# Kernel tuning notes

Measured on AMD Instinct MI355X. Metric: run time of the kernel, lower is better.

Reference implementation:

```python
import jax, jax.numpy as jnp
import numpy as np

N = 50000          # num nodes
E = 600000         # num edges
F_IN = 128         # num_features
H = 128            # graph_hidden_dim
R = 2              # num_relations
L = 3              # n_layers_conv
BN_EPS = 1e-5
BN_BETA = 1e-4     # BatchNorm bias init per module code


def setup_inputs() -> dict:
    key = jax.random.key(0)
    ks = jax.random.split(key, 9)
    s_in = 1.0 / np.sqrt(F_IN)
    s_h = 1.0 / np.sqrt(H)
    return {
        "x": jax.random.normal(ks[0], (N, F_IN), jnp.float32),
        "edge_index": jax.random.randint(ks[1], (2, E), 0, N, jnp.int32),
        "edge_type": jax.random.randint(ks[2], (E,), 0, R, jnp.int32),
        "W0_rel": jax.random.normal(ks[3], (R, F_IN, H), jnp.float32) * s_in,
        "W0_root": jax.random.normal(ks[4], (F_IN, H), jnp.float32) * s_in,
        "b0": jnp.zeros((H,), jnp.float32),
        "Ws_rel": jax.random.normal(ks[5], (L, R, H, H), jnp.float32) * s_h,
        "Ws_root": jax.random.normal(ks[6], (L, H, H), jnp.float32) * s_h,
        "bs": jnp.zeros((L, H), jnp.float32),
    }


def batchnorm(x):
    # training-mode BatchNorm1d over nodes; weight=1, bias=1e-4 (per init)
    mu = jnp.mean(x, axis=0)
    var = jnp.mean((x - mu) ** 2, axis=0)  # biased var, as torch uses for norm
    return (x - mu) * jax.lax.rsqrt(var + BN_EPS) + BN_BETA


def rgcn_conv(x, src, dst, edge_type, W_rel, W_root, b):
    # PyG RGCNConv, aggr='mean': per-relation mean of x[src] at dst,
    # then per-relation linear, plus root transform and bias.
    seg = dst * R + edge_type  # combined (node, relation) segment id
    msgs = x[src]                                   # [E, d] gather
    sums = jax.ops.segment_sum(msgs, seg, num_segments=N * R)
    cnts = jax.ops.segment_sum(jnp.ones((src.shape[0],), x.dtype), seg,
                               num_segments=N * R)
    mean = sums.reshape(N, R, -1) / jnp.maximum(cnts, 1.0).reshape(N, R, 1)
    out = jnp.einsum('nrd,rdh->nh', mean, W_rel) + x @ W_root + b
    return out


def reference(x, edge_index, edge_type, W0_rel, W0_root, b0, Ws_rel, Ws_root, bs):
    src, dst = edge_index[0], edge_index[1]
    h = batchnorm(x)
    h = jax.nn.relu(rgcn_conv(h, src, dst, edge_type, W0_rel, W0_root, b0))
    for i in range(L):
        h_ = batchnorm(h)
        h_ = jax.nn.relu(rgcn_conv(h_, src, dst, edge_type,
                                   Ws_rel[i], Ws_root[i], bs[i]))
        h = h + h_  # conv_residual=True
    return h  # gconv_dropout == 0
```

## Files before the change

kernel.cpp:

```cpp
#include <hip/hip_runtime.h>
#include <hip/hip_bf16.h>

#define N_NODES 50000
#define N_EDGES 600000
#define F 128
#define R 2
#define NLAYER 4
#define NSEG (N_NODES * R)
#define SEGP (NSEG / 8)
#define NSCB 98
#define NB 384
#define BN_EPS 1e-5f
#define BETA 1e-4f

typedef __hip_bfloat16 bf16;
typedef __attribute__((ext_vector_type(8))) short short8;
typedef __attribute__((ext_vector_type(4))) short short4x;
typedef __attribute__((ext_vector_type(4))) float floatx4;

__device__ __forceinline__ float b2f(short s) {
    union { unsigned u; float f; } c;
    c.u = ((unsigned)(unsigned short)s) << 16;
    return c.f;
}

__global__ void k_wt(const float* __restrict__ W0_rel, const float* __restrict__ W0_root,
                     const float* __restrict__ Ws_rel, const float* __restrict__ Ws_root,
                     bf16* __restrict__ Bt) {
    int idx = blockIdx.x * 256 + threadIdx.x;
    if (idx >= NLAYER * NB * F) return;
    int l = idx / (NB * F);
    int rem = idx % (NB * F);
    int j = rem / F, d = rem % F;
    float v;
    if (j < 256) {
        int r = j >> 7, c = j & 127;
        v = (l == 0) ? W0_rel[(r * F + d) * F + c]
                     : Ws_rel[((size_t)((l - 1) * R + r) * F + d) * F + c];
    } else {
        int c = j - 256;
        v = (l == 0) ? W0_root[d * F + c]
                     : Ws_root[((size_t)(l - 1) * F + d) * F + c];
    }
    Bt[idx] = __float2bfloat16(v);
}

__global__ void k_seg(const int* __restrict__ dst, const int* __restrict__ et,
                      int* __restrict__ seg) {
    int e = blockIdx.x * 256 + threadIdx.x;
    if (e < N_EDGES) seg[e] = dst[e] * R + et[e];
}

__global__ void k_count(const int* __restrict__ seg, int* __restrict__ cnt) {
    int g = blockIdx.x & 7;
    int lo = g * SEGP, hi = lo + SEGP;
    for (int e = (blockIdx.x >> 3) * 256 + threadIdx.x; e < N_EDGES; e += 65536) {
        int s = seg[e];
        if (s >= lo && s < hi) atomicAdd(&cnt[s], 1);
    }
}

__global__ void k_scan1(const int* __restrict__ cnt, int* __restrict__ off,
                        int* __restrict__ bsum) {
    int t = threadIdx.x;
    int g = blockIdx.x * 1024 + t;
    int v = (g < NSEG) ? cnt[g] : 0;
    int lane = t & 63;
    int wv = t >> 6;
    int x = v;
    for (int d = 1; d < 64; d <<= 1) {
        int y = __shfl_up(x, d, 64);
        if (lane >= d) x += y;
    }
    __shared__ int wtot[16];
    if (lane == 63) wtot[wv] = x;
    __syncthreads();
    if (t < 16) {
        int s = wtot[t];
        for (int d = 1; d < 16; d <<= 1) {
            int y = __shfl_up(s, d, 64);
            if (t >= d) s += y;
        }
        wtot[t] = s;
    }
    __syncthreads();
    int wpre = (wv == 0) ? 0 : wtot[wv - 1];
    int incl = x + wpre;
    if (g < NSEG) off[g] = incl - v;
    if (t == 1023) bsum[blockIdx.x] = incl;
}

__global__ void k_scan2(int* __restrict__ bsum) {
    __shared__ int s[128];
    int t = threadIdx.x;
    int v = (t < NSCB) ? bsum[t] : 0;
    s[t] = v;
    __syncthreads();
    for (int d = 1; d < 128; d <<= 1) {
        int y = (t >= d) ? s[t - d] : 0;
        __syncthreads();
        s[t] += y;
        __syncthreads();
    }
    if (t < NSCB) bsum[t] = s[t] - v;
}

__global__ void k_scan3(int* __restrict__ off, const int* __restrict__ bsum) {
    int g = blockIdx.x * 1024 + threadIdx.x;
    if (g < NSEG) off[g] += bsum[blockIdx.x];
}

__global__ void k_fill(const int* __restrict__ src, const int* __restrict__ seg,
                       const int* __restrict__ off,
                       int* __restrict__ fill, int* __restrict__ esrc) {
    int g = blockIdx.x & 7;
    int lo = g * SEGP, hi = lo + SEGP;
    for (int e = (blockIdx.x >> 3) * 256 + threadIdx.x; e < N_EDGES; e += 65536) {
        int s = seg[e];
        if (s >= lo && s < hi) {
            int idx = off[s] + atomicAdd(&fill[s], 1);
            esrc[idx] = src[e];
        }
    }
}

__global__ void k_bnstats(const float* __restrict__ h, float* __restrict__ gs) {
    int c = threadIdx.x & 127;
    int rl = threadIdx.x >> 7;
    float s = 0.f, q = 0.f;
    for (int r = blockIdx.x * 2 + rl; r < N_NODES; r += gridDim.x * 2) {
        float v = h[(size_t)r * F + c];
        s += v; q += v * v;
    }
    __shared__ float ls[256], lq[256];
    ls[threadIdx.x] = s; lq[threadIdx.x] = q;
    __syncthreads();
    if (rl == 0) {
        atomicAdd(&gs[c], ls[c] + ls[c + 128]);
        atomicAdd(&gs[128 + c], lq[c] + lq[c + 128]);
    }
}

__launch_bounds__(512)
__global__ void k_gemm(const float* __restrict__ h, const float* __restrict__ gs,
                       const bf16* __restrict__ Bt, const float* __restrict__ bias,
                       bf16* __restrict__ y, bf16* __restrict__ z) {
    __shared__ bf16 As[64 * 136];
    __shared__ bf16 Bs[128 * 136];
    int t = threadIdx.x;
    int m0 = blockIdx.x * 64;
    int c4 = (t & 31) * 4;
    float mu[4], rs[4];
    for (int c = 0; c < 4; c++) {
        float mm = gs[c4 + c] * (1.0f / N_NODES);
        float qq = gs[128 + c4 + c] * (1.0f / N_NODES);
        mu[c] = mm;
        rs[c] = rsqrtf(qq - mm * mm + BN_EPS);
    }
    int r0 = t >> 5;
    for (int it = 0; it < 4; it++) {
        int row = r0 + it * 16;
        int m = m0 + row;
        float4 v = {0.f, 0.f, 0.f, 0.f};
        if (m < N_NODES) v = *(const float4*)(h + (size_t)m * F + c4);
        bf16 o[4];
        o[0] = __float2bfloat16((v.x - mu[0]) * rs[0] + BETA);
        o[1] = __float2bfloat16((v.y - mu[1]) * rs[1] + BETA);
        o[2] = __float2bfloat16((v.z - mu[2]) * rs[2] + BETA);
        o[3] = __float2bfloat16((v.w - mu[3]) * rs[3] + BETA);
        *(double*)(As + row * 136 + c4) = *(const double*)o;
    }
    __syncthreads();
    int w = t >> 6;
    int lane = t & 63;
    int msub = w & 3;
    int nh = w >> 2;
    int lm = lane & 15;
    int lq = lane >> 4;
    short8 a[4];
    for (int ki = 0; ki < 4; ki++)
        a[ki] = *(const short8*)(As + (msub * 16 + lm) * 136 + ki * 32 + lq * 8);
    int m = m0 + msub * 16 + lm;
    for (int ci = 0; ci < 3; ci++) {
        __syncthreads();
        {
            const bf16* bsrc = Bt + (size_t)ci * 128 * F;
            for (int rr = 0; rr < 4; rr++) {
                int idx = rr * 512 + t;
                int row = idx >> 4;
                int kc = idx & 15;
                short8 v = *(const short8*)(bsrc + row * F + kc * 8);
                *(short8*)(Bs + row * 136 + kc * 8) = v;
            }
        }
        __syncthreads();
        for (int tt = 0; tt < 4; tt++) {
            int nt = nh * 4 + tt;
            short8 b[4];
            for (int ki = 0; ki < 4; ki++)
                b[ki] = *(const short8*)(Bs + (nt * 16 + lm) * 136 + ki * 32 + lq * 8);
            floatx4 acc = {0.f, 0.f, 0.f, 0.f};
            for (int ki = 0; ki < 4; ki++)
                acc = __builtin_amdgcn_mfma_f32_16x16x32_bf16(b[ki], a[ki], acc, 0, 0, 0);
            int n0 = ci * 128 + nt * 16 + lq * 4;
            if (m < N_NODES) {
                if (ci < 2) {
                    union { bf16 o[4]; double d; } u;
                    u.o[0] = __float2bfloat16(acc[0]);
                    u.o[1] = __float2bfloat16(acc[1]);
                    u.o[2] = __float2bfloat16(acc[2]);
                    u.o[3] = __float2bfloat16(acc[3]);
                    *(double*)(y + (size_t)m * 256 + n0) = u.d;
                } else {
                    float4 bv = *(const float4*)(bias + (n0 - 256));
                    union { bf16 o[4]; double d; } u;
                    u.o[0] = __float2bfloat16(acc[0] + bv.x);
                    u.o[1] = __float2bfloat16(acc[1] + bv.y);
                    u.o[2] = __float2bfloat16(acc[2] + bv.z);
                    u.o[3] = __float2bfloat16(acc[3] + bv.w);
                    *(double*)(z + (size_t)m * F + (n0 - 256)) = u.d;
                }
            }
        }
    }
}

__global__ void k_aggregate(const bf16* __restrict__ y, const bf16* __restrict__ z,
                            const int* __restrict__ cnt, const int* __restrict__ off,
                            const int* __restrict__ esrc,
                            const float* __restrict__ hres, float* __restrict__ hout,
                            int layer) {
    int wid = (blockIdx.x * 256 + threadIdx.x) >> 6;
    int lane = threadIdx.x & 63;
    if (wid >= N_NODES) return;
    int n = wid;
    int half = lane >> 5;
    int hl = lane & 31;
    int c4 = hl * 4;
    int2 cc = *(const int2*)(cnt + n * R);
    int o0 = off[n * R];
    int myc = half ? cc.y : cc.x;
    int myo = half ? (o0 + cc.x) : o0;
    float myinv = (myc > 0) ? 1.0f / (float)myc : 0.f;
    const bf16* yb = y + half * 128 + c4;
    float s0 = 0.f, s1 = 0.f, s2 = 0.f, s3 = 0.f;
    for (int i = 0; i < myc; i += 8) {
        int sn[8];
        #pragma unroll
        for (int k = 0; k < 8; k++) {
            int valid = (i + k < myc);
            sn[k] = esrc[valid ? (myo + i + k) : myo];
        }
        short4x p[8];
        #pragma unroll
        for (int k = 0; k < 8; k++)
            p[k] = *(const short4x*)(yb + (size_t)sn[k] * 256);
        #pragma unroll
        for (int k = 0; k < 8; k++) {
            float wk = (i + k < myc) ? myinv : 0.f;
            s0 = fmaf(b2f(p[k].x), wk, s0);
            s1 = fmaf(b2f(p[k].y), wk, s1);
            s2 = fmaf(b2f(p[k].z), wk, s2);
            s3 = fmaf(b2f(p[k].w), wk, s3);
        }
    }
    float t0 = __shfl_xor(s0, 32, 64);
    float t1 = __shfl_xor(s1, 32, 64);
    float t2 = __shfl_xor(s2, 32, 64);
    float t3 = __shfl_xor(s3, 32, 64);
    if (half == 0) {
        short4x zb = *(const short4x*)(z + (size_t)n * F + c4);
        float4 hp = {0.f, 0.f, 0.f, 0.f};
        if (layer > 0) hp = *(const float4*)(hres + (size_t)n * F + c4);
        float4 o4;
        o4.x = fmaxf(b2f(zb.x) + s0 + t0, 0.f) + hp.x;
        o4.y = fmaxf(b2f(zb.y) + s1 + t1, 0.f) + hp.y;
        o4.z = fmaxf(b2f(zb.z) + s2 + t2, 0.f) + hp.z;
        o4.w = fmaxf(b2f(zb.w) + s3 + t3, 0.f) + hp.w;
        *(float4*)(hout + (size_t)n * F + c4) = o4;
    }
}

extern "C" void kernel_launch(void* const* d_in, const int* in_sizes, int n_in,
                              void* d_out, int out_size, void* d_ws, size_t ws_size,
                              hipStream_t stream) {
    const float* x       = (const float*)d_in[0];
    const int*   eidx    = (const int*)d_in[1];
    const int*   etype   = (const int*)d_in[2];
    const float* W0_rel  = (const float*)d_in[3];
    const float* W0_root = (const float*)d_in[4];
    const float* b0      = (const float*)d_in[5];
    const float* Ws_rel  = (const float*)d_in[6];
    const float* Ws_root = (const float*)d_in[7];
    const float* bs      = (const float*)d_in[8];
    const int* src = eidx;
    const int* dst = eidx + N_EDGES;

    char* w = (char*)d_ws;
    float* h   = (float*)w; w += (size_t)N_NODES * F * 4;
    bf16*  z   = (bf16*)w;  w += (size_t)N_NODES * F * 2;
    bf16*  y   = (bf16*)w;  w += (size_t)N_NODES * 256 * 2;
    bf16*  Bt  = (bf16*)w;  w += (size_t)NLAYER * NB * F * 2;
    int* cnt   = (int*)w;   w += (size_t)NSEG * 4;
    int* fill  = (int*)w;   w += (size_t)NSEG * 4;
    float* stats = (float*)w; w += (size_t)NLAYER * 256 * 4;
    int* off   = (int*)w;   w += (size_t)NSEG * 4;
    int* esrc  = (int*)w;   w += (size_t)N_EDGES * 4;
    int* segb  = (int*)w;   w += (size_t)N_EDGES * 4;
    int* bsum  = (int*)w;   w += 128 * 4;

    hipMemsetAsync(cnt, 0, (size_t)NSEG * 4 * 2 + (size_t)NLAYER * 256 * 4, stream);
    k_wt<<<(NLAYER * NB * F + 255) / 256, 256, 0, stream>>>(W0_rel, W0_root, Ws_rel, Ws_root, Bt);
    k_seg<<<(N_EDGES + 255) / 256, 256, 0, stream>>>(dst, etype, segb);
    k_count<<<2048, 256, 0, stream>>>(segb, cnt);
    k_scan1<<<NSCB, 1024, 0, stream>>>(cnt, off, bsum);
    k_scan2<<<1, 128, 0, stream>>>(bsum);
    k_scan3<<<NSCB, 1024, 0, stream>>>(off, bsum);
    k_fill<<<2048, 256, 0, stream>>>(src, segb, off, fill, esrc);

    for (int l = 0; l < NLAYER; l++) {
        float* gs = stats + l * 256;
        const float* bias = (l == 0) ? b0 : (bs + (size_t)(l - 1) * F);
        const float* hin = (l == 0) ? x : h;
        k_bnstats<<<512, 256, 0, stream>>>(hin, gs);
        k_gemm<<<(N_NODES + 63) / 64, 512, 0, stream>>>(
            hin, gs, Bt + (size_t)l * NB * F, bias, y, z);
        k_aggregate<<<(N_NODES * 64 + 255) / 256, 256, 0, stream>>>(
            y, z, cnt, off, esrc, h, (l == 3) ? (float*)d_out : h, l);
    }
}
```

Measured before the change: 473.1 us.

## Fuse next-layer BatchNorm statistics into aggregate epilogue with sharded atomics

Each aggregate kernel now accumulates per-column sum and sum-of-squares of its output for the next layer's BatchNorm. It reduces these in shared memory per block and atomically adds them into one of 8 sharded stat buffers. This drops three separate k_bnstats passes that each re-read the full hidden state. The GEMM sums the 8 shards when computing mean and rstd. In exchange it adds a __syncthreads and many global float atomics per aggregate block, which may contend.

```diff
diff --git a/kernel.cpp b/kernel.cpp
--- a/kernel.cpp
+++ b/kernel.cpp
@@ -10,6 +10,7 @@
 #define SEGP (NSEG / 8)
 #define NSCB 98
 #define NB 384
+#define STATS_STRIDE 2048
 #define BN_EPS 1e-5f
 #define BETA 1e-4f
 
@@ -152,8 +153,14 @@
     int c4 = (t & 31) * 4;
     float mu[4], rs[4];
     for (int c = 0; c < 4; c++) {
-        float mm = gs[c4 + c] * (1.0f / N_NODES);
-        float qq = gs[128 + c4 + c] * (1.0f / N_NODES);
+        float ssum = 0.f, qsum = 0.f;
+        #pragma unroll
+        for (int k = 0; k < 8; k++) {
+            ssum += gs[k * 256 + c4 + c];
+            qsum += gs[k * 256 + 128 + c4 + c];
+        }
+        float mm = ssum * (1.0f / N_NODES);
+        float qq = qsum * (1.0f / N_NODES);
         mu[c] = mm;
         rs[c] = rsqrtf(qq - mm * mm + BN_EPS);
     }
@@ -229,10 +236,9 @@
                             const int* __restrict__ cnt, const int* __restrict__ off,
                             const int* __restrict__ esrc,
                             const float* __restrict__ hres, float* __restrict__ hout,
-                            int layer) {
+                            float* __restrict__ gs_next, int layer) {
     int wid = (blockIdx.x * 256 + threadIdx.x) >> 6;
     int lane = threadIdx.x & 63;
-    if (wid >= N_NODES) return;
     int n = wid;
     int half = lane >> 5;
     int hl = lane & 31;
@@ -268,6 +274,8 @@
     float t1 = __shfl_xor(s1, 32, 64);
     float t2 = __shfl_xor(s2, 32, 64);
     float t3 = __shfl_xor(s3, 32, 64);
+    __shared__ float ls[4][128], lq[4][128];
+    int wv = threadIdx.x >> 6;
     if (half == 0) {
         short4x zb = *(const short4x*)(z + (size_t)n * F + c4);
         float4 hp = {0.f, 0.f, 0.f, 0.f};
@@ -278,6 +286,25 @@
         o4.z = fmaxf(b2f(zb.z) + s2 + t2, 0.f) + hp.z;
         o4.w = fmaxf(b2f(zb.w) + s3 + t3, 0.f) + hp.w;
         *(float4*)(hout + (size_t)n * F + c4) = o4;
+        if (gs_next) {
+            ls[wv][c4 + 0] = o4.x; ls[wv][c4 + 1] = o4.y;
+            ls[wv][c4 + 2] = o4.z; ls[wv][c4 + 3] = o4.w;
+            lq[wv][c4 + 0] = o4.x * o4.x; lq[wv][c4 + 1] = o4.y * o4.y;
+            lq[wv][c4 + 2] = o4.z * o4.z; lq[wv][c4 + 3] = o4.w * o4.w;
+        }
+    }
+    if (gs_next) {
+        __syncthreads();
+        int t = threadIdx.x;
+        float* gsc = gs_next + (blockIdx.x & 7) * 256;
+        if (t < 128) {
+            float S = (ls[0][t] + ls[1][t]) + (ls[2][t] + ls[3][t]);
+            atomicAdd(&gsc[t], S);
+        } else if (t < 256) {
+            int c = t - 128;
+            float Q = (lq[0][c] + lq[1][c]) + (lq[2][c] + lq[3][c]);
+            atomicAdd(&gsc[128 + c], Q);
+        }
     }
 }
 
@@ -303,13 +330,13 @@
     bf16*  Bt  = (bf16*)w;  w += (size_t)NLAYER * NB * F * 2;
     int* cnt   = (int*)w;   w += (size_t)NSEG * 4;
     int* fill  = (int*)w;   w += (size_t)NSEG * 4;
-    float* stats = (float*)w; w += (size_t)NLAYER * 256 * 4;
+    float* stats = (float*)w; w += (size_t)NLAYER * STATS_STRIDE * 4;
     int* off   = (int*)w;   w += (size_t)NSEG * 4;
     int* esrc  = (int*)w;   w += (size_t)N_EDGES * 4;
     int* segb  = (int*)w;   w += (size_t)N_EDGES * 4;
     int* bsum  = (int*)w;   w += 128 * 4;
 
-    hipMemsetAsync(cnt, 0, (size_t)NSEG * 4 * 2 + (size_t)NLAYER * 256 * 4, stream);
+    hipMemsetAsync(cnt, 0, (size_t)NSEG * 4 * 2 + (size_t)NLAYER * STATS_STRIDE * 4, stream);
     k_wt<<<(NLAYER * NB * F + 255) / 256, 256, 0, stream>>>(W0_rel, W0_root, Ws_rel, Ws_root, Bt);
     k_seg<<<(N_EDGES + 255) / 256, 256, 0, stream>>>(dst, etype, segb);
     k_count<<<2048, 256, 0, stream>>>(segb, cnt);
@@ -317,15 +344,16 @@
     k_scan2<<<1, 128, 0, stream>>>(bsum);
     k_scan3<<<NSCB, 1024, 0, stream>>>(off, bsum);
     k_fill<<<2048, 256, 0, stream>>>(src, segb, off, fill, esrc);
+    k_bnstats<<<512, 256, 0, stream>>>(x, stats);
 
     for (int l = 0; l < NLAYER; l++) {
-        float* gs = stats + l * 256;
+        const float* gsl = stats + (size_t)l * STATS_STRIDE;
         const float* bias = (l == 0) ? b0 : (bs + (size_t)(l - 1) * F);
         const float* hin = (l == 0) ? x : h;
-        k_bnstats<<<512, 256, 0, stream>>>(hin, gs);
         k_gemm<<<(N_NODES + 63) / 64, 512, 0, stream>>>(
-            hin, gs, Bt + (size_t)l * NB * F, bias, y, z);
+            hin, gsl, Bt + (size_t)l * NB * F, bias, y, z);
         k_aggregate<<<(N_NODES * 64 + 255) / 256, 256, 0, stream>>>(
-            y, z, cnt, off, esrc, h, (l == 3) ? (float*)d_out : h, l);
-    }
-}
+            y, z, cnt, off, esrc, h, (l == 3) ? (float*)d_out : h,
+            (l < 3) ? (float*)(stats + (size_t)(l + 1) * STATS_STRIDE) : nullptr, l);
+    }
+}
```

Measured after the change: 449.9 us. 1.05x faster.
